# Kernel optimization log

Hardware: AMD Instinct MI355X
Metric: run time of the kernel (lower is better)

Reference implementation:

```python
import jax, jax.numpy as jnp
import numpy as np

SIZES = [256, 512, 1024, 2048, 4096]
EPS = 1e-6


def setup_inputs() -> dict:
    key = jax.random.key(0)
    x = jax.random.normal(key, (4, 4096, 4096), dtype=jnp.float32)
    scale = jnp.ones((4096,), dtype=jnp.float32)
    return {"x": x, "scale": scale}


def reference(x, scale):
    # Single cumulative sum-of-squares pass replaces the per-prefix mean
    # recomputation in the original loop (same math: mean = cumsum[s-1]/s).
    cs = jnp.cumsum(x * x, axis=-1)  # [B, S, D]
    segs = []
    prev = 0
    for s in SIZES:  # small fixed list of nested sizes
        rrms = jax.lax.rsqrt(cs[..., s - 1 : s] / s + EPS)  # [B, S, 1]
        segs.append(x[..., prev:s] * rrms)
        prev = s
    out = jnp.concatenate(segs, axis=-1)  # [B, S, D]
    return out * scale
```

## Files before the change

### kernel.cpp

```cpp
#include <hip/hip_runtime.h>


#define D 4096

typedef float f32x4 __attribute__((ext_vector_type(4)));

__global__ __launch_bounds__(256) void mrms_kernel(
    const float* __restrict__ x,
    const float* __restrict__ scale,
    float* __restrict__ out)
{
    const int row = blockIdx.x;
    const size_t base = (size_t)row * D;
    const f32x4* __restrict__ xr  = reinterpret_cast<const f32x4*>(x + base);
    f32x4* __restrict__ outr      = reinterpret_cast<f32x4*>(out + base);
    const f32x4* __restrict__ sc4 = reinterpret_cast<const f32x4*>(scale);

    const int t = threadIdx.x;

    f32x4 v0 = __builtin_nontemporal_load(&xr[t]);
    f32x4 v1 = __builtin_nontemporal_load(&xr[t + 256]);
    f32x4 v2 = __builtin_nontemporal_load(&xr[t + 512]);
    f32x4 v3 = __builtin_nontemporal_load(&xr[t + 768]);
    f32x4 g0 = sc4[t];
    f32x4 g1 = sc4[t + 256];
    f32x4 g2 = sc4[t + 512];
    f32x4 g3 = sc4[t + 768];

    float a = v0.x*v0.x + v0.y*v0.y + v0.z*v0.z + v0.w*v0.w;
    float b = v1.x*v1.x + v1.y*v1.y + v1.z*v1.z + v1.w*v1.w;
    float c = v2.x*v2.x + v2.y*v2.y + v2.z*v2.z + v2.w*v2.w
            + v3.x*v3.x + v3.y*v3.y + v3.z*v3.z + v3.w*v3.w;

    #pragma unroll
    for (int off = 32; off > 0; off >>= 1) {
        a += __shfl_down(a, off, 64);
        b += __shfl_down(b, off, 64);
        c += __shfl_down(c, off, 64);
    }

    __shared__ float lds[4][3];
    const int wave = t >> 6;
    if ((t & 63) == 0) {
        lds[wave][0] = a;
        lds[wave][1] = b;
        lds[wave][2] = c;
    }
    __syncthreads();

    const float seg0 = lds[0][0];
    const float seg1 = lds[1][0];
    const float seg2 = lds[2][0] + lds[3][0];
    const float seg3 = lds[0][1] + lds[1][1] + lds[2][1] + lds[3][1];
    const float seg4 = lds[0][2] + lds[1][2] + lds[2][2] + lds[3][2];

    const float cum0 = seg0;
    const float cum1 = cum0 + seg1;
    const float cum2 = cum1 + seg2;
    const float cum3 = cum2 + seg3;
    const float cum4 = cum3 + seg4;

    const float EPS = 1e-6f;
    const float r0 = rsqrtf(cum0 * (1.0f / 256.0f)  + EPS);
    const float r1 = rsqrtf(cum1 * (1.0f / 512.0f)  + EPS);
    const float r2 = rsqrtf(cum2 * (1.0f / 1024.0f) + EPS);
    const float r3 = rsqrtf(cum3 * (1.0f / 2048.0f) + EPS);
    const float r4 = rsqrtf(cum4 * (1.0f / 4096.0f) + EPS);

    const float rc0 = (t < 64) ? r0 : ((t < 128) ? r1 : r2);

    f32x4 o;
    o.x = v0.x * rc0 * g0.x;  o.y = v0.y * rc0 * g0.y;
    o.z = v0.z * rc0 * g0.z;  o.w = v0.w * rc0 * g0.w;
    __builtin_nontemporal_store(o, &outr[t]);

    o.x = v1.x * r3 * g1.x;   o.y = v1.y * r3 * g1.y;
    o.z = v1.z * r3 * g1.z;   o.w = v1.w * r3 * g1.w;
    __builtin_nontemporal_store(o, &outr[t + 256]);

    o.x = v2.x * r4 * g2.x;   o.y = v2.y * r4 * g2.y;
    o.z = v2.z * r4 * g2.z;   o.w = v2.w * r4 * g2.w;
    __builtin_nontemporal_store(o, &outr[t + 512]);

    o.x = v3.x * r4 * g3.x;   o.y = v3.y * r4 * g3.y;
    o.z = v3.z * r4 * g3.z;   o.w = v3.w * r4 * g3.w;
    __builtin_nontemporal_store(o, &outr[t + 768]);
}

extern "C" void kernel_launch(void* const* d_in, const int* in_sizes, int n_in,
                              void* d_out, int out_size, void* d_ws, size_t ws_size,
                              hipStream_t stream) {
    const float* x     = (const float*)d_in[0];
    const float* scale = (const float*)d_in[1];
    float* out         = (float*)d_out;

    const int nrows = in_sizes[0] / D;
    mrms_kernel<<<nrows, 256, 0, stream>>>(x, scale, out);
}
```

Measured before the change: 414.4 us.

## Map one wavefront per row and reduce with wave shuffles only

Each 64-lane wavefront now handles a whole 4096-element row, 16 float4 chunks per lane, and each block covers four rows. The prefix sums of squares are reduced entirely with xor shuffles inside the wave, which removes the LDS exchange and the block-wide barrier. The x loads are also switched from nontemporal to ordinary loads. In exchange, register pressure rises sharply (v and g together hold 128 floats per lane), which may cut occupancy and leave fewer loads in flight to hide memory latency.

```diff
diff --git a/kernel.cpp b/kernel.cpp
--- a/kernel.cpp
+++ b/kernel.cpp
@@ -10,55 +10,46 @@
     const float* __restrict__ scale,
     float* __restrict__ out)
 {
-    const int row = blockIdx.x;
+    const int lane = threadIdx.x & 63;
+    const int row  = blockIdx.x * 4 + (threadIdx.x >> 6);
     const size_t base = (size_t)row * D;
-    const f32x4* __restrict__ xr  = reinterpret_cast<const f32x4*>(x + base);
-    f32x4* __restrict__ outr      = reinterpret_cast<f32x4*>(out + base);
-    const f32x4* __restrict__ sc4 = reinterpret_cast<const f32x4*>(scale);
+    const f32x4* __restrict__ xr   = reinterpret_cast<const f32x4*>(x + base);
+    f32x4* __restrict__ outr       = reinterpret_cast<f32x4*>(out + base);
+    const f32x4* __restrict__ sc4  = reinterpret_cast<const f32x4*>(scale);
 
-    const int t = threadIdx.x;
+    f32x4 v[16];
+    #pragma unroll
+    for (int c = 0; c < 16; ++c) v[c] = xr[c * 64 + lane];
+    f32x4 g[16];
+    #pragma unroll
+    for (int c = 0; c < 16; ++c) g[c] = sc4[c * 64 + lane];
 
-    f32x4 v0 = __builtin_nontemporal_load(&xr[t]);
-    f32x4 v1 = __builtin_nontemporal_load(&xr[t + 256]);
-    f32x4 v2 = __builtin_nontemporal_load(&xr[t + 512]);
-    f32x4 v3 = __builtin_nontemporal_load(&xr[t + 768]);
-    f32x4 g0 = sc4[t];
-    f32x4 g1 = sc4[t + 256];
-    f32x4 g2 = sc4[t + 512];
-    f32x4 g3 = sc4[t + 768];
+    float ss[16];
+    #pragma unroll
+    for (int c = 0; c < 16; ++c)
+        ss[c] = v[c].x*v[c].x + v[c].y*v[c].y + v[c].z*v[c].z + v[c].w*v[c].w;
 
-    float a = v0.x*v0.x + v0.y*v0.y + v0.z*v0.z + v0.w*v0.w;
-    float b = v1.x*v1.x + v1.y*v1.y + v1.z*v1.z + v1.w*v1.w;
-    float c = v2.x*v2.x + v2.y*v2.y + v2.z*v2.z + v2.w*v2.w
-            + v3.x*v3.x + v3.y*v3.y + v3.z*v3.z + v3.w*v3.w;
+    float a0 = ss[0];
+    float a1 = ss[1];
+    float a2 = ss[2] + ss[3];
+    float a3 = (ss[4] + ss[5]) + (ss[6] + ss[7]);
+    float a4 = ((ss[8] + ss[9]) + (ss[10] + ss[11]))
+             + ((ss[12] + ss[13]) + (ss[14] + ss[15]));
 
     #pragma unroll
-    for (int off = 32; off > 0; off >>= 1) {
-        a += __shfl_down(a, off, 64);
-        b += __shfl_down(b, off, 64);
-        c += __shfl_down(c, off, 64);
+    for (int off = 1; off < 64; off <<= 1) {
+        a0 += __shfl_xor(a0, off, 64);
+        a1 += __shfl_xor(a1, off, 64);
+        a2 += __shfl_xor(a2, off, 64);
+        a3 += __shfl_xor(a3, off, 64);
+        a4 += __shfl_xor(a4, off, 64);
     }
 
-    __shared__ float lds[4][3];
-    const int wave = t >> 6;
-    if ((t & 63) == 0) {
-        lds[wave][0] = a;
-        lds[wave][1] = b;
-        lds[wave][2] = c;
-    }
-    __syncthreads();
-
-    const float seg0 = lds[0][0];
-    const float seg1 = lds[1][0];
-    const float seg2 = lds[2][0] + lds[3][0];
-    const float seg3 = lds[0][1] + lds[1][1] + lds[2][1] + lds[3][1];
-    const float seg4 = lds[0][2] + lds[1][2] + lds[2][2] + lds[3][2];
-
-    const float cum0 = seg0;
-    const float cum1 = cum0 + seg1;
-    const float cum2 = cum1 + seg2;
-    const float cum3 = cum2 + seg3;
-    const float cum4 = cum3 + seg4;
+    const float cum0 = a0;
+    const float cum1 = cum0 + a1;
+    const float cum2 = cum1 + a2;
+    const float cum3 = cum2 + a3;
+    const float cum4 = cum3 + a4;
 
     const float EPS = 1e-6f;
     const float r0 = rsqrtf(cum0 * (1.0f / 256.0f)  + EPS);
@@ -67,24 +58,19 @@
     const float r3 = rsqrtf(cum3 * (1.0f / 2048.0f) + EPS);
     const float r4 = rsqrtf(cum4 * (1.0f / 4096.0f) + EPS);
 
-    const float rc0 = (t < 64) ? r0 : ((t < 128) ? r1 : r2);
+    const float rr[16] = { r0, r1, r2, r2,
+                           r3, r3, r3, r3,
+                           r4, r4, r4, r4, r4, r4, r4, r4 };
 
-    f32x4 o;
-    o.x = v0.x * rc0 * g0.x;  o.y = v0.y * rc0 * g0.y;
-    o.z = v0.z * rc0 * g0.z;  o.w = v0.w * rc0 * g0.w;
-    __builtin_nontemporal_store(o, &outr[t]);
-
-    o.x = v1.x * r3 * g1.x;   o.y = v1.y * r3 * g1.y;
-    o.z = v1.z * r3 * g1.z;   o.w = v1.w * r3 * g1.w;
-    __builtin_nontemporal_store(o, &outr[t + 256]);
-
-    o.x = v2.x * r4 * g2.x;   o.y = v2.y * r4 * g2.y;
-    o.z = v2.z * r4 * g2.z;   o.w = v2.w * r4 * g2.w;
-    __builtin_nontemporal_store(o, &outr[t + 512]);
-
-    o.x = v3.x * r4 * g3.x;   o.y = v3.y * r4 * g3.y;
-    o.z = v3.z * r4 * g3.z;   o.w = v3.w * r4 * g3.w;
-    __builtin_nontemporal_store(o, &outr[t + 768]);
+    #pragma unroll
+    for (int c = 0; c < 16; ++c) {
+        f32x4 o;
+        o.x = v[c].x * rr[c] * g[c].x;
+        o.y = v[c].y * rr[c] * g[c].y;
+        o.z = v[c].z * rr[c] * g[c].z;
+        o.w = v[c].w * rr[c] * g[c].w;
+        __builtin_nontemporal_store(o, &outr[c * 64 + lane]);
+    }
 }
 
 extern "C" void kernel_launch(void* const* d_in, const int* in_sizes, int n_in,
@@ -95,5 +81,5 @@
     float* out         = (float*)d_out;
 
     const int nrows = in_sizes[0] / D;
-    mrms_kernel<<<nrows, 256, 0, stream>>>(x, scale, out);
+    mrms_kernel<<<nrows / 4, 256, 0, stream>>>(x, scale, out);
 }
```

Measured after the change: 446.2 us. 1.08x slower.
